# Kernel tuning notes

Measured on AMD Instinct MI355X. Metric: run time of the kernel, lower is better.

Reference implementation:

```python
import jax, jax.numpy as jnp
import numpy as np

L, H, P = 16384, 1024, 512
DT_MIN, DT_MAX = 1e-3, 1e-1
STEP_RESCALE = 1.0


def setup_inputs() -> dict:
    key = jax.random.key(0)
    ks = jax.random.split(key, 7)
    input_sequence = jax.random.normal(ks[0], (L, H), jnp.float32)
    # eigenvalues with negative real part (left half plane), HiPPO-like imag parts
    Lambda_re = -(jax.random.uniform(ks[1], (P,), jnp.float32) * 0.9 + 0.1)
    Lambda_im = jnp.pi * jnp.arange(P, dtype=jnp.float32)
    B = jax.random.normal(ks[2], (P, H, 2), jnp.float32) / jnp.sqrt(2.0 * H)   # real/imag of B_tilde (P,H)
    C = jax.random.normal(ks[3], (H, P, 2), jnp.float32) / jnp.sqrt(2.0 * P)   # real/imag of C_tilde (H,P)
    D = jax.random.normal(ks[4], (H,), jnp.float32)
    u01 = jax.random.uniform(ks[5], (P, 1), jnp.float32)
    log_step = jnp.log(DT_MIN) + u01 * (jnp.log(DT_MAX) - jnp.log(DT_MIN))     # (P,1)
    return dict(input_sequence=input_sequence, Lambda_re=Lambda_re, Lambda_im=Lambda_im,
                B=B, C=C, D=D, log_step=log_step)


def _binop(q_i, q_j):
    # diagonal linear recurrence composition: (A, b) pairs
    A_i, b_i = q_i
    A_j, b_j = q_j
    return A_j * A_i, A_j * b_i + b_j


def reference(input_sequence, Lambda_re, Lambda_im, B, C, D, log_step):
    Lambda = Lambda_re + 1j * Lambda_im                        # (P,) complex64
    B_tilde = B[..., 0] + 1j * B[..., 1]                       # (P,H)
    C_tilde = C[..., 0] + 1j * C[..., 1]                       # (H,P)
    step = STEP_RESCALE * jnp.exp(log_step[:, 0])              # (P,)
    # ZOH discretization
    Lambda_bar = jnp.exp(Lambda * step)                        # (P,)
    B_bar = ((Lambda_bar - 1.0) / Lambda)[:, None] * B_tilde   # (P,H)
    # Bu_elements: (L,P) complex
    Bu = input_sequence.astype(B_bar.dtype) @ B_bar.T
    Lambda_elems = jnp.broadcast_to(Lambda_bar, Bu.shape)      # (L,P)
    # parallel associative scan over the diagonal recurrence x_t = Lambda_bar*x_{t-1} + Bu_t
    _, xs = jax.lax.associative_scan(_binop, (Lambda_elems, Bu))
    ys = 2.0 * (xs @ C_tilde.T).real                           # conj_sym => factor 2, (L,H)
    return ys + D * input_sequence
```

## Files before the change

### kernel.cpp

```cpp
#include <hip/hip_runtime.h>
#include <math.h>

#define L_SEQ 16384
#define H_DIM 1024
#define P_DIM 512
#define N2P   1024
#define KDIM  1024
#define NKT   16
#define CHUNK 64
#define NCHUNK 256

typedef __attribute__((ext_vector_type(8))) short short8;
typedef __attribute__((ext_vector_type(4))) float f32x4;

__device__ __forceinline__ unsigned short f2bf(float f){
    unsigned int u = __float_as_uint(f);
    u = (u + 0x7FFFu + ((u >> 16) & 1u)) >> 16;
    return (unsigned short)u;
}
__device__ __forceinline__ float bf2f(unsigned int lo16){
    return __uint_as_float(lo16 << 16);
}

__global__ void k_prep_lambda(const float* __restrict__ lre, const float* __restrict__ lim,
                              const float* __restrict__ lstep,
                              float* __restrict__ lam, float* __restrict__ coef,
                              float* __restrict__ lpow)
{
    int p = threadIdx.x;
    double step = exp((double)lstep[p]);
    double dr = (double)lre[p], di = (double)lim[p];
    double ar = dr*step, ai = di*step;
    double er = exp(ar);
    double lbr = er*cos(ai), lbi = er*sin(ai);
    lam[2*p] = (float)lbr; lam[2*p+1] = (float)lbi;
    double nr = lbr - 1.0, ni = lbi;
    double d2 = dr*dr + di*di;
    coef[2*p]   = (float)((nr*dr + ni*di)/d2);
    coef[2*p+1] = (float)((ni*dr - nr*di)/d2);
    double xr = lbr, xi = lbi;
    #pragma unroll
    for (int s=0;s<6;s++){ double t = xr*xr - xi*xi; xi = 2.0*xr*xi; xr = t; }
    lpow[2*p] = (float)xr; lpow[2*p+1] = (float)xi;
}

__global__ __launch_bounds__(256)
void k_prep_bc(const float* __restrict__ B, const float* __restrict__ C,
               const float* __restrict__ coef,
               unsigned short* __restrict__ BB, unsigned short* __restrict__ CC)
{
    int bid = blockIdx.x;
    if (bid < 2048){
        int i = bid*256 + threadIdx.x;
        int p = i >> 10, h = i & 1023;
        float br = B[2*i], bi = B[2*i+1];
        float cr = coef[2*p], ci = coef[2*p+1];
        BB[(size_t)(2*p)*H_DIM + h]   = f2bf(cr*br - ci*bi);
        BB[(size_t)(2*p+1)*H_DIM + h] = f2bf(cr*bi + ci*br);
    } else {
        int i = (bid-2048)*256 + threadIdx.x;
        int h = i >> 9, p = i & 511;
        float cr = C[2*i], ci = C[2*i+1];
        CC[(size_t)h*N2P + 2*p]     = f2bf(2.f*cr);
        CC[(size_t)h*N2P + 2*p + 1] = f2bf(-2.f*ci);
    }
}

template<int CAST>
__global__ __launch_bounds__(256, 2)
void gemm128(const unsigned short* __restrict__ A16, const float* __restrict__ A32,
             const unsigned short* __restrict__ Bm,
             float* __restrict__ Cf, unsigned short* __restrict__ Cb,
             const float* __restrict__ Dv, const float* __restrict__ U32)
{
    __shared__ char lds[65536];
    const int tid  = threadIdx.x;
    const int lane = tid & 63;
    const int wid  = tid >> 6;
    const int wm = wid >> 1, wn = wid & 1;
    const int wg = ((int)blockIdx.x & 7) * 128 + ((int)blockIdx.x >> 3);
    const int tm = wg >> 3, tn = wg & 7;
    const int lr = lane & 15;

    const int srow = tid >> 3;
    const int sch  = (tid & 7) ^ ((tid >> 3) & 7);
    const int scol = sch << 3;
    const int kc0 = (((lane >> 4)      ^ (lr & 7)) << 4);
    const int kc1 = ((((lane >> 4) | 4) ^ (lr & 7)) << 4);
    const int aOff = (wm*64 + lr)*128;
    const int bOff = 16384 + (wn*64 + lr)*128;

#define GLOAD(SRC, DST) __builtin_amdgcn_global_load_lds( \
        (const __attribute__((address_space(1))) void*)(SRC), \
        (__attribute__((address_space(3))) void*)(DST), 16, 0, 0)
#define RD(OFF) (*(const short8*)(lds + (OFF)))
#define MFMA(a,b,c) __builtin_amdgcn_mfma_f32_16x16x32_bf16(a,b,c,0,0,0)

    auto stage_b = [&](int kt_){
        char* d_ = lds + ((kt_&1)<<15) + 16384 + tid*16;
        const unsigned short* sb = Bm + (size_t)(tn*128 + srow)*KDIM + (size_t)kt_*64 + scol;
        GLOAD(sb,                    d_);
        GLOAD(sb + (size_t)32*KDIM,  d_ + 4096);
        GLOAD(sb + (size_t)64*KDIM,  d_ + 8192);
        GLOAD(sb + (size_t)96*KDIM,  d_ + 12288);
    };
    auto stage_a16 = [&](int kt_){
        char* d_ = lds + ((kt_&1)<<15) + tid*16;
        const unsigned short* sa = A16 + (size_t)(tm*128 + srow)*KDIM + (size_t)kt_*64 + scol;
        GLOAD(sa,                    d_);
        GLOAD(sa + (size_t)32*KDIM,  d_ + 4096);
        GLOAD(sa + (size_t)64*KDIM,  d_ + 8192);
        GLOAD(sa + (size_t)96*KDIM,  d_ + 12288);
    };

    f32x4 acc[4][4];
    #pragma unroll
    for (int m=0;m<4;m++)
        #pragma unroll
        for (int n=0;n<4;n++) acc[m][n] = (f32x4){0.f,0.f,0.f,0.f};

    float4 av[4][2];
    auto load_a32 = [&](int kt_){
        #pragma unroll
        for (int g=0; g<4; ++g){
            const float* sa = A32 + (size_t)(tm*128 + g*32 + srow)*KDIM + (size_t)kt_*64 + scol;
            av[g][0] = *reinterpret_cast<const float4*>(sa);
            av[g][1] = *reinterpret_cast<const float4*>(sa + 4);
        }
    };
    auto write_a32 = [&](int kt_){
        #pragma unroll
        for (int g=0; g<4; ++g){
            union { short8 v; unsigned short s[8]; } r;
            r.s[0]=f2bf(av[g][0].x); r.s[1]=f2bf(av[g][0].y);
            r.s[2]=f2bf(av[g][0].z); r.s[3]=f2bf(av[g][0].w);
            r.s[4]=f2bf(av[g][1].x); r.s[5]=f2bf(av[g][1].y);
            r.s[6]=f2bf(av[g][1].z); r.s[7]=f2bf(av[g][1].w);
            *reinterpret_cast<short8*>(lds + ((kt_&1)<<15) + g*4096 + tid*16) = r.v;
        }
    };

    if (CAST){ load_a32(0); write_a32(0); } else { stage_a16(0); }
    stage_b(0);
    __syncthreads();

    for (int kt = 0; kt < NKT; ++kt) {
        const int sb = (kt & 1) << 15;
        const int tN = (kt + 1) & (NKT - 1);
        if (CAST) load_a32(tN); else stage_a16(tN);
        stage_b(tN);

        short8 a0[4], b0[4], a1v[4], b1v[4];
        #pragma unroll
        for (int m=0;m<4;m++) a0[m]  = RD(sb + aOff + m*2048 + kc0);
        #pragma unroll
        for (int n=0;n<4;n++) b0[n]  = RD(sb + bOff + n*2048 + kc0);
        #pragma unroll
        for (int m=0;m<4;m++) a1v[m] = RD(sb + aOff + m*2048 + kc1);
        #pragma unroll
        for (int n=0;n<4;n++) b1v[n] = RD(sb + bOff + n*2048 + kc1);
        #pragma unroll
        for (int m=0;m<4;m++)
            #pragma unroll
            for (int n=0;n<4;n++) acc[m][n] = MFMA(a0[m], b0[n], acc[m][n]);
        #pragma unroll
        for (int m=0;m<4;m++)
            #pragma unroll
            for (int n=0;n<4;n++) acc[m][n] = MFMA(a1v[m], b1v[n], acc[m][n]);

        if (CAST) write_a32(tN);
        __syncthreads();
    }

    const int orow0 = tm*128 + wm*64 + (lane>>4)*4;
    const int ocol0 = tn*128 + wn*64 + lr;
    #pragma unroll
    for (int m=0;m<4;m++){
        #pragma unroll
        for (int n=0;n<4;n++){
            int row = orow0 + m*16, col = ocol0 + n*16;
            #pragma unroll
            for (int j=0;j<4;j++){
                size_t idx = (size_t)(row + j)*N2P + col;
                if (CAST) Cb[idx] = f2bf(acc[m][n][j]);
                else      Cf[idx] = acc[m][n][j] + Dv[col]*U32[idx];
            }
        }
    }
#undef GLOAD
#undef RD
#undef MFMA
}

__global__ __launch_bounds__(512)
void k_agg(const unsigned int* __restrict__ Bu, const float* __restrict__ lam,
           float* __restrict__ agg)
{
    int p = threadIdx.x, c = blockIdx.x;
    float lrr = lam[2*p], lii = lam[2*p+1];
    float xr = 0.f, xi = 0.f;
    const unsigned int* b2 = Bu + (size_t)c*CHUNK*512 + p;
    #pragma unroll 4
    for (int t=0;t<CHUNK;t++){
        unsigned int b = b2[(size_t)t*512];
        float br = __uint_as_float(b << 16);
        float bi = __uint_as_float(b & 0xffff0000u);
        float tr = lrr*xr - lii*xi + br;
        xi = lrr*xi + lii*xr + bi;
        xr = tr;
    }
    agg[((size_t)c*P_DIM + p)*2]     = xr;
    agg[((size_t)c*P_DIM + p)*2 + 1] = xi;
}

__global__ __launch_bounds__(256)
void k_scan(const float* __restrict__ agg, const float* __restrict__ lpow,
            float* __restrict__ xinit)
{
    __shared__ float sr[NCHUNK], si[NCHUNK];
    int c = threadIdx.x, p = blockIdx.x;
    float xr = agg[((size_t)c*P_DIM + p)*2];
    float xi = agg[((size_t)c*P_DIM + p)*2 + 1];
    sr[c] = xr; si[c] = xi;
    float wr = lpow[2*p], wi = lpow[2*p+1];
    for (int s=1; s<NCHUNK; s<<=1){
        __syncthreads();
        float ur = 0.f, ui = 0.f;
        if (c >= s){ ur = sr[c-s]; ui = si[c-s]; }
        __syncthreads();
        xr += wr*ur - wi*ui;
        xi += wr*ui + wi*ur;
        sr[c] = xr; si[c] = xi;
        float t = wr*wr - wi*wi; wi = 2.f*wr*wi; wr = t;
    }
    __syncthreads();
    float er = 0.f, ei = 0.f;
    if (c > 0){ er = sr[c-1]; ei = si[c-1]; }
    xinit[((size_t)c*P_DIM + p)*2]     = er;
    xinit[((size_t)c*P_DIM + p)*2 + 1] = ei;
}

__global__ __launch_bounds__(512)
void k_apply(const unsigned int* __restrict__ Bu, const float* __restrict__ lam,
             const float* __restrict__ xinit, unsigned int* __restrict__ xs)
{
    int p = threadIdx.x, c = blockIdx.x;
    float lrr = lam[2*p], lii = lam[2*p+1];
    float xr = xinit[((size_t)c*P_DIM + p)*2];
    float xi = xinit[((size_t)c*P_DIM + p)*2 + 1];
    const unsigned int* b2 = Bu + (size_t)c*CHUNK*512 + p;
    unsigned int* o = xs + (size_t)c*CHUNK*512 + p;
    #pragma unroll 4
    for (int t=0;t<CHUNK;t++){
        unsigned int b = b2[(size_t)t*512];
        float br = __uint_as_float(b << 16);
        float bi = __uint_as_float(b & 0xffff0000u);
        float tr = lrr*xr - lii*xi + br;
        xi = lrr*xi + lii*xr + bi;
        xr = tr;
        o[(size_t)t*512] = (unsigned int)f2bf(xr) | ((unsigned int)f2bf(xi) << 16);
    }
}

extern "C" void kernel_launch(void* const* d_in, const int* in_sizes, int n_in,
                              void* d_out, int out_size, void* d_ws, size_t ws_size,
                              hipStream_t stream)
{
    const float* u   = (const float*)d_in[0];
    const float* lre = (const float*)d_in[1];
    const float* lim = (const float*)d_in[2];
    const float* B   = (const float*)d_in[3];
    const float* C   = (const float*)d_in[4];
    const float* D   = (const float*)d_in[5];
    const float* ls  = (const float*)d_in[6];
    float* out = (float*)d_out;

    char* w = (char*)d_ws;
    unsigned short* xs16 = (unsigned short*)(w + 0);
    unsigned short* Bu16 = (unsigned short*)(w + 33554432);
    unsigned short* BB   = (unsigned short*)(w + 67108864);
    unsigned short* CC   = (unsigned short*)(w + 69206016);
    float* lam   = (float*)(w + 71303168);
    float* coef  = (float*)(w + 71307264);
    float* lpow  = (float*)(w + 71311360);
    float* agg   = (float*)(w + 71315456);
    float* xinit = (float*)(w + 72364032);

    k_prep_lambda<<<1, P_DIM, 0, stream>>>(lre, lim, ls, lam, coef, lpow);
    k_prep_bc<<<4096, 256, 0, stream>>>(B, C, coef, BB, CC);

    gemm128<1><<<1024, 256, 0, stream>>>(nullptr, u, BB, nullptr, Bu16, nullptr, nullptr);

    k_agg<<<NCHUNK, P_DIM, 0, stream>>>((const unsigned int*)Bu16, lam, agg);
    k_scan<<<P_DIM, NCHUNK, 0, stream>>>(agg, lpow, xinit);
    k_apply<<<NCHUNK, P_DIM, 0, stream>>>((const unsigned int*)Bu16, lam, xinit,
                                          (unsigned int*)xs16);

    gemm128<0><<<1024, 256, 0, stream>>>(xs16, nullptr, CC, out, nullptr, D, u);
}
```

Baseline: 152.3 us.

## Switch GEMM to four-slot K=32 LDS ring with single barrier per step

Rewrites the bf16 MFMA GEMM main loop to use a 4-deep ring of 16KB LDS slots with K-tiles of 32, prefetching two tiles ahead. Each step uses one raw s_barrier with explicit vmcnt/lgkmcnt waits instead of a full __syncthreads. The LDS swizzle is changed to match. The goal is to hide global-load latency better and cut barrier overhead. In exchange it doubles the number of loop iterations, halves MFMA work per barrier, and relies on hand-tuned waitcnt counts, which carries a correctness risk around ring-slot reuse.

```diff
diff --git a/kernel.cpp b/kernel.cpp
--- a/kernel.cpp
+++ b/kernel.cpp
@@ -6,7 +6,7 @@
 #define P_DIM 512
 #define N2P   1024
 #define KDIM  1024
-#define NKT   16
+#define NKT2  32
 #define CHUNK 64
 #define NCHUNK 256
 
@@ -17,9 +17,6 @@
     unsigned int u = __float_as_uint(f);
     u = (u + 0x7FFFu + ((u >> 16) & 1u)) >> 16;
     return (unsigned short)u;
-}
-__device__ __forceinline__ float bf2f(unsigned int lo16){
-    return __uint_as_float(lo16 << 16);
 }
 
 __global__ void k_prep_lambda(const float* __restrict__ lre, const float* __restrict__ lim,
@@ -82,95 +79,95 @@
     const int tm = wg >> 3, tn = wg & 7;
     const int lr = lane & 15;
 
-    const int srow = tid >> 3;
-    const int sch  = (tid & 7) ^ ((tid >> 3) & 7);
-    const int scol = sch << 3;
-    const int kc0 = (((lane >> 4)      ^ (lr & 7)) << 4);
-    const int kc1 = ((((lane >> 4) | 4) ^ (lr & 7)) << 4);
-    const int aOff = (wm*64 + lr)*128;
-    const int bOff = 16384 + (wn*64 + lr)*128;
+    const int srow = tid >> 2;
+    const int scol = ((tid & 3) ^ ((tid >> 3) & 3)) << 3;
+    const int kc   = (((lane >> 4) ^ ((lr >> 1) & 3)) << 4);
+    const int aOff = wm*4096 + lr*64 + kc;
+    const int bOff = 8192 + wn*4096 + lr*64 + kc;
 
 #define GLOAD(SRC, DST) __builtin_amdgcn_global_load_lds( \
         (const __attribute__((address_space(1))) void*)(SRC), \
         (__attribute__((address_space(3))) void*)(DST), 16, 0, 0)
 #define RD(OFF) (*(const short8*)(lds + (OFF)))
 #define MFMA(a,b,c) __builtin_amdgcn_mfma_f32_16x16x32_bf16(a,b,c,0,0,0)
-
-    auto stage_b = [&](int kt_){
-        char* d_ = lds + ((kt_&1)<<15) + 16384 + tid*16;
-        const unsigned short* sb = Bm + (size_t)(tn*128 + srow)*KDIM + (size_t)kt_*64 + scol;
-        GLOAD(sb,                    d_);
-        GLOAD(sb + (size_t)32*KDIM,  d_ + 4096);
-        GLOAD(sb + (size_t)64*KDIM,  d_ + 8192);
-        GLOAD(sb + (size_t)96*KDIM,  d_ + 12288);
-    };
-    auto stage_a16 = [&](int kt_){
-        char* d_ = lds + ((kt_&1)<<15) + tid*16;
-        const unsigned short* sa = A16 + (size_t)(tm*128 + srow)*KDIM + (size_t)kt_*64 + scol;
-        GLOAD(sa,                    d_);
-        GLOAD(sa + (size_t)32*KDIM,  d_ + 4096);
-        GLOAD(sa + (size_t)64*KDIM,  d_ + 8192);
-        GLOAD(sa + (size_t)96*KDIM,  d_ + 12288);
-    };
-
-    f32x4 acc[4][4];
-    #pragma unroll
-    for (int m=0;m<4;m++)
-        #pragma unroll
-        for (int n=0;n<4;n++) acc[m][n] = (f32x4){0.f,0.f,0.f,0.f};
-
-    float4 av[4][2];
+#define ABAR  asm volatile("s_barrier" ::: "memory")
+
+    auto stage_b = [&](int kt_, int slot_){
+        char* d_ = lds + (slot_<<14) + 8192 + tid*16;
+        const unsigned short* sb = Bm + (size_t)(tn*128 + srow)*KDIM + (size_t)kt_*32 + scol;
+        GLOAD(sb,                   d_);
+        GLOAD(sb + (size_t)64*KDIM, d_ + 4096);
+    };
+    auto stage_a16 = [&](int kt_, int slot_){
+        char* d_ = lds + (slot_<<14) + tid*16;
+        const unsigned short* sa = A16 + (size_t)(tm*128 + srow)*KDIM + (size_t)kt_*32 + scol;
+        GLOAD(sa,                   d_);
+        GLOAD(sa + (size_t)64*KDIM, d_ + 4096);
+    };
+    float4 av[2][2];
     auto load_a32 = [&](int kt_){
         #pragma unroll
-        for (int g=0; g<4; ++g){
-            const float* sa = A32 + (size_t)(tm*128 + g*32 + srow)*KDIM + (size_t)kt_*64 + scol;
+        for (int g=0; g<2; ++g){
+            const float* sa = A32 + (size_t)(tm*128 + g*64 + srow)*KDIM + (size_t)kt_*32 + scol;
             av[g][0] = *reinterpret_cast<const float4*>(sa);
             av[g][1] = *reinterpret_cast<const float4*>(sa + 4);
         }
     };
-    auto write_a32 = [&](int kt_){
-        #pragma unroll
-        for (int g=0; g<4; ++g){
+    auto write_a32 = [&](int slot_){
+        #pragma unroll
+        for (int g=0; g<2; ++g){
             union { short8 v; unsigned short s[8]; } r;
             r.s[0]=f2bf(av[g][0].x); r.s[1]=f2bf(av[g][0].y);
             r.s[2]=f2bf(av[g][0].z); r.s[3]=f2bf(av[g][0].w);
             r.s[4]=f2bf(av[g][1].x); r.s[5]=f2bf(av[g][1].y);
             r.s[6]=f2bf(av[g][1].z); r.s[7]=f2bf(av[g][1].w);
-            *reinterpret_cast<short8*>(lds + ((kt_&1)<<15) + g*4096 + tid*16) = r.v;
-        }
-    };
-
-    if (CAST){ load_a32(0); write_a32(0); } else { stage_a16(0); }
-    stage_b(0);
-    __syncthreads();
-
-    for (int kt = 0; kt < NKT; ++kt) {
-        const int sb = (kt & 1) << 15;
-        const int tN = (kt + 1) & (NKT - 1);
-        if (CAST) load_a32(tN); else stage_a16(tN);
-        stage_b(tN);
-
-        short8 a0[4], b0[4], a1v[4], b1v[4];
-        #pragma unroll
-        for (int m=0;m<4;m++) a0[m]  = RD(sb + aOff + m*2048 + kc0);
-        #pragma unroll
-        for (int n=0;n<4;n++) b0[n]  = RD(sb + bOff + n*2048 + kc0);
-        #pragma unroll
-        for (int m=0;m<4;m++) a1v[m] = RD(sb + aOff + m*2048 + kc1);
-        #pragma unroll
-        for (int n=0;n<4;n++) b1v[n] = RD(sb + bOff + n*2048 + kc1);
+            *reinterpret_cast<short8*>(lds + (slot_<<14) + g*4096 + tid*16) = r.v;
+        }
+    };
+
+    f32x4 acc[4][4];
+    #pragma unroll
+    for (int m=0;m<4;m++)
+        #pragma unroll
+        for (int n=0;n<4;n++) acc[m][n] = (f32x4){0.f,0.f,0.f,0.f};
+
+    if (CAST){
+        load_a32(0); stage_b(0,0); write_a32(0);
+        load_a32(1); stage_b(1,1); write_a32(1);
+        asm volatile("s_waitcnt lgkmcnt(0)" ::: "memory");
+    } else {
+        stage_a16(0,0); stage_b(0,0); stage_a16(1,1); stage_b(1,1);
+    }
+
+    #pragma unroll 4
+    for (int kt = 0; kt < NKT2; ++kt) {
+        const int sb   = (kt & 3) << 14;
+        const int slot = (kt + 2) & 3;
+        const int tt   = (kt+2 < NKT2) ? kt+2 : NKT2-1;
+        if (CAST){
+            load_a32(tt);
+            stage_b(tt, slot);
+            asm volatile("s_waitcnt lgkmcnt(0)" ::: "memory");
+        } else {
+            stage_a16(tt, slot);
+            stage_b(tt, slot);
+            asm volatile("s_waitcnt vmcnt(8)" ::: "memory");
+        }
+        ABAR;
+
+        short8 afr[4], bfr[4];
+        #pragma unroll
+        for (int m=0;m<4;m++) afr[m] = RD(sb + aOff + m*1024);
+        #pragma unroll
+        for (int n=0;n<4;n++) bfr[n] = RD(sb + bOff + n*1024);
         #pragma unroll
         for (int m=0;m<4;m++)
             #pragma unroll
-            for (int n=0;n<4;n++) acc[m][n] = MFMA(a0[m], b0[n], acc[m][n]);
-        #pragma unroll
-        for (int m=0;m<4;m++)
-            #pragma unroll
-            for (int n=0;n<4;n++) acc[m][n] = MFMA(a1v[m], b1v[n], acc[m][n]);
-
-        if (CAST) write_a32(tN);
-        __syncthreads();
-    }
+            for (int n=0;n<4;n++) acc[m][n] = MFMA(afr[m], bfr[n], acc[m][n]);
+
+        if (CAST) write_a32(slot);
+    }
+    asm volatile("s_waitcnt vmcnt(0) lgkmcnt(0)" ::: "memory");
 
     const int orow0 = tm*128 + wm*64 + (lane>>4)*4;
     const int ocol0 = tn*128 + wn*64 + lr;
@@ -190,6 +187,7 @@
 #undef GLOAD
 #undef RD
 #undef MFMA
+#undef ABAR
 }
 
 __global__ __launch_bounds__(512)
```

Result: slower. 155.5 us (+2.1%).

## Prefetch two K-tiles ahead with manual waitcnt and raw barriers in GEMM

Applied to the files above, without the earlier changes.

Restructures the GEMM main loop to issue global-to-LDS loads two K-tiles ahead, not one. It replaces __syncthreads with explicit s_waitcnt vmcnt/lgkmcnt plus raw s_barrier, so outstanding async loads can stay in flight across the barrier. New loads go out only after the fragment reads into registers, and the MFMAs then overlap with those loads. This relies on the LDS double buffer still being safe with depth-two prefetch and on hand-counted vmcnt values, which are fragile and a race risk.

```diff
diff --git a/kernel.cpp b/kernel.cpp
--- a/kernel.cpp
+++ b/kernel.cpp
@@ -17,9 +17,6 @@
     unsigned int u = __float_as_uint(f);
     u = (u + 0x7FFFu + ((u >> 16) & 1u)) >> 16;
     return (unsigned short)u;
-}
-__device__ __forceinline__ float bf2f(unsigned int lo16){
-    return __uint_as_float(lo16 << 16);
 }
 
 __global__ void k_prep_lambda(const float* __restrict__ lre, const float* __restrict__ lim,
@@ -83,8 +80,7 @@
     const int lr = lane & 15;
 
     const int srow = tid >> 3;
-    const int sch  = (tid & 7) ^ ((tid >> 3) & 7);
-    const int scol = sch << 3;
+    const int scol = ((tid & 7) ^ ((tid >> 3) & 7)) << 3;
     const int kc0 = (((lane >> 4)      ^ (lr & 7)) << 4);
     const int kc1 = ((((lane >> 4) | 4) ^ (lr & 7)) << 4);
     const int aOff = (wm*64 + lr)*128;
@@ -95,6 +91,7 @@
         (__attribute__((address_space(3))) void*)(DST), 16, 0, 0)
 #define RD(OFF) (*(const short8*)(lds + (OFF)))
 #define MFMA(a,b,c) __builtin_amdgcn_mfma_f32_16x16x32_bf16(a,b,c,0,0,0)
+#define ABAR  asm volatile("s_barrier" ::: "memory")
 
     auto stage_b = [&](int kt_){
         char* d_ = lds + ((kt_&1)<<15) + 16384 + tid*16;
@@ -112,13 +109,6 @@
         GLOAD(sa + (size_t)64*KDIM,  d_ + 8192);
         GLOAD(sa + (size_t)96*KDIM,  d_ + 12288);
     };
-
-    f32x4 acc[4][4];
-    #pragma unroll
-    for (int m=0;m<4;m++)
-        #pragma unroll
-        for (int n=0;n<4;n++) acc[m][n] = (f32x4){0.f,0.f,0.f,0.f};
-
     float4 av[4][2];
     auto load_a32 = [&](int kt_){
         #pragma unroll
@@ -140,15 +130,30 @@
         }
     };
 
-    if (CAST){ load_a32(0); write_a32(0); } else { stage_a16(0); }
-    stage_b(0);
-    __syncthreads();
+    f32x4 acc[4][4];
+    #pragma unroll
+    for (int m=0;m<4;m++)
+        #pragma unroll
+        for (int n=0;n<4;n++) acc[m][n] = (f32x4){0.f,0.f,0.f,0.f};
+
+    if (CAST){
+        load_a32(0); write_a32(0); stage_b(0);
+        load_a32(1); write_a32(1); stage_b(1);
+        asm volatile("s_waitcnt lgkmcnt(0)" ::: "memory");
+    } else {
+        stage_a16(0); stage_b(0); stage_a16(1); stage_b(1);
+    }
 
     for (int kt = 0; kt < NKT; ++kt) {
         const int sb = (kt & 1) << 15;
-        const int tN = (kt + 1) & (NKT - 1);
-        if (CAST) load_a32(tN); else stage_a16(tN);
-        stage_b(tN);
+        const int tt = (kt+2 < NKT) ? kt+2 : NKT-1;
+        if (CAST){
+            load_a32(tt);
+            asm volatile("s_waitcnt vmcnt(12)" ::: "memory");
+        } else {
+            asm volatile("s_waitcnt vmcnt(8)" ::: "memory");
+        }
+        ABAR;
 
         short8 a0[4], b0[4], a1v[4], b1v[4];
         #pragma unroll
@@ -159,6 +164,14 @@
         for (int m=0;m<4;m++) a1v[m] = RD(sb + aOff + m*2048 + kc1);
         #pragma unroll
         for (int n=0;n<4;n++) b1v[n] = RD(sb + bOff + n*2048 + kc1);
+        asm volatile("s_waitcnt lgkmcnt(0)" ::: "memory");
+        ABAR;
+
+        if (CAST){
+            stage_b(tt);
+        } else {
+            stage_a16(tt); stage_b(tt);
+        }
         #pragma unroll
         for (int m=0;m<4;m++)
             #pragma unroll
@@ -167,10 +180,9 @@
         for (int m=0;m<4;m++)
             #pragma unroll
             for (int n=0;n<4;n++) acc[m][n] = MFMA(a1v[m], b1v[n], acc[m][n]);
-
-        if (CAST) write_a32(tN);
-        __syncthreads();
-    }
+        if (CAST) write_a32(tt);
+    }
+    asm volatile("s_waitcnt vmcnt(0) lgkmcnt(0)" ::: "memory");
 
     const int orow0 = tm*128 + wm*64 + (lane>>4)*4;
     const int ocol0 = tn*128 + wn*64 + lr;
@@ -190,6 +202,7 @@
 #undef GLOAD
 #undef RD
 #undef MFMA
+#undef ABAR
 }
 
 __global__ __launch_bounds__(512)
```

New measurement: 140.4 us. -7.8%, faster.
